# Performance work log

Measured on AMD Instinct MI355X. Metric: run time of the kernel, lower is better.

The kernel has to match this reference:

```python
import jax, jax.numpy as jnp
import numpy as np

POOLING_COUNTS = [15, 8, 8]
N_GRID = 64


def _build_plan(pooling_counts, n):
    """Return list of (kernel_size, conv_stride, i_idx, j_idx) matching torch module order."""
    plan = []
    stride, offset = 1, 0
    for gi, c in enumerate(pooling_counts):
        for k in range(c):
            offset += stride
            i = np.arange(0, n - offset, stride)
            j = np.arange(offset, n, stride)
            ksz = 3 if (gi > 0 and k == 0) else 2
            cstride = 2 if ksz == 3 else 1
            plan.append((ksz, cstride, i, j))
        stride *= 2
    return plan


def _conv1d(x, w, b, stride):
    # x: [B, C, L], w: [O, I, K]
    y = jax.lax.conv_general_dilated(
        x, w, window_strides=(stride,), padding='VALID',
        dimension_numbers=('NCH', 'OIH', 'NCH'))
    return y + b[None, :, None]


def setup_inputs() -> dict:
    key = jax.random.key(0)
    ks = jax.random.split(key, 5)
    H = 256
    x = jax.random.normal(ks[0], (32, H, N_GRID), dtype=jnp.float32)
    w2 = jax.random.normal(ks[1], (29, H, H, 2), dtype=jnp.float32) * 0.03
    b2 = jnp.zeros((29, H), dtype=jnp.float32)
    w3 = jax.random.normal(ks[2], (2, H, H, 3), dtype=jnp.float32) * 0.03
    b3 = jnp.zeros((2, H), dtype=jnp.float32)
    vis_w = jax.random.normal(ks[3], (H, 3 * H), dtype=jnp.float32) * 0.03
    vis_b = jnp.zeros((H,), dtype=jnp.float32)
    return {"x": x, "w2": w2, "b2": b2, "w3": w3, "b3": b3,
            "vis_w": vis_w, "vis_b": vis_b}


def reference(x, w2, b2, w3, b3, vis_w, vis_b):
    plan = _build_plan(POOLING_COUNTS, N_GRID)
    B, D, n = x.shape
    diag = np.arange(n)
    src = x
    map2d = jnp.zeros((B, 3 * D, n, n), dtype=x.dtype)
    map2d = map2d.at[:, :, diag, diag].set(jnp.tile(x, (1, 3, 1)))
    cur = x
    i2 = i3 = 0
    for ksz, cstride, ii, jj in plan:
        if ksz == 2:
            w, b = w2[i2], b2[i2]; i2 += 1
        else:
            w, b = w3[i3], b3[i3]; i3 += 1
        cur = _conv1d(cur, w, b, cstride)          # [B, D, len(ii)]
        feat = jnp.concatenate([src[:, :, ii], cur, src[:, :, jj]], axis=1)
        map2d = map2d.at[:, :, ii, jj].set(feat)
    # 1x1 Conv2d(3D -> D)
    out = jnp.einsum('bcij,oc->boij', map2d, vis_w) + vis_b[None, :, None, None]
    return out
```

## Files before the change

kernel.cpp:

```cpp
#include <hip/hip_runtime.h>

#define BB 32
#define NSTEP 31
#define CROW 1040
#define CB_STRIDE 266240L
#define XB_STRIDE 16384L
#define PPART 524288L
#define RS 528
#define BUF (64 * RS)

__device__ __constant__ int d_lens[NSTEP] = {63,62,61,60,59,58,57,56,55,54,53,52,51,50,49,
                                             24,23,22,21,20,19,18,17,
                                             8,7,6,5,4,3,2,1};
__device__ __constant__ int d_cb[NSTEP] = {0,63,125,186,246,305,363,420,476,531,585,638,690,741,791,
                                           840,864,887,909,930,950,969,987,
                                           1004,1012,1019,1025,1030,1034,1037,1039};

typedef short v8s __attribute__((ext_vector_type(8)));
typedef float v4f __attribute__((ext_vector_type(4)));

__device__ __forceinline__ unsigned short rne_bf16(float f) {
    unsigned int u = __float_as_uint(f);
    u = (u + 0x7FFFu + ((u >> 16) & 1u)) >> 16;
    return (unsigned short)u;
}

#define MFMA16 __builtin_amdgcn_mfma_f32_16x16x32_bf16

__device__ __forceinline__ void lds_barrier() {
    asm volatile("s_waitcnt lgkmcnt(0)\n\ts_barrier" ::: "memory");
}

__global__ __launch_bounds__(256)
void prep(const float* __restrict__ x, const float* __restrict__ w2,
          const float* __restrict__ w3, const float* __restrict__ vw,
          unsigned short* __restrict__ xb, unsigned short* __restrict__ w2t,
          unsigned short* __restrict__ w3t, unsigned short* __restrict__ vwb)
{
    long idx = (long)blockIdx.x * 256 + threadIdx.x;
    if (idx < 524288) {
        const int ci = idx & 255, l = (idx >> 8) & 63, b = (int)(idx >> 14);
        xb[idx] = rne_bf16(x[((long)b << 14) + ((long)ci << 6) + l]);
        return;
    }
    idx -= 524288;
    if (idx < 3801088) {
        const int ci = idx & 255, k = (idx >> 8) & 1; const long row = idx >> 9;
        w2t[idx] = rne_bf16(w2[row * 512 + ci * 2 + k]);
        return;
    }
    idx -= 3801088;
    if (idx < 393216) {
        const int ci = idx & 255; const long r = idx >> 8;
        const int k = (int)(r % 3); const long row = r / 3;
        w3t[idx] = rne_bf16(w3[row * 768 + ci * 3 + k]);
        return;
    }
    idx -= 393216;
    if (idx < 196608) vwb[idx] = rne_bf16(vw[idx]);
}


template<int KC, int S>
__device__ __forceinline__ void conv_big(
    const unsigned short* __restrict__ Wt, const float* __restrict__ bias,
    const char* in, char* out, unsigned short* __restrict__ Cbp,
    int L, int wave, int nl, int g)
{
    const int wm = wave >> 1;
    const int lg2 = wave & 1;
    const int l0 = lg2 * 32 + nl, l1 = l0 + 16;
    const int lv0 = min(l0, L - 1), lv1 = min(l1, L - 1);

    v4f a00 = {0,0,0,0}, a01 = {0,0,0,0}, a10 = {0,0,0,0}, a11 = {0,0,0,0};
    const unsigned short* A0 = Wt + (size_t)(wm * 32 + nl) * (KC * 256) + g * 8;
    const unsigned short* A1 = A0 + (size_t)16 * (KC * 256);

    #pragma unroll
    for (int c = 0; c < KC; ++c) {
        v8s wf0[8], wf1[8];
        #pragma unroll
        for (int k = 0; k < 8; ++k) {
            wf0[k] = *(const v8s*)(A0 + (c * 8 + k) * 32);
            wf1[k] = *(const v8s*)(A1 + (c * 8 + k) * 32);
        }
        const char* rp0 = in + (lv0 * S + c) * RS + g * 16;
        const char* rp1 = in + (lv1 * S + c) * RS + g * 16;
        #pragma unroll
        for (int k = 0; k < 8; ++k) {
            const v8s b0 = *(const v8s*)(rp0 + k * 64);
            const v8s b1 = *(const v8s*)(rp1 + k * 64);
            a00 = MFMA16(wf0[k], b0, a00, 0, 0, 0);
            a10 = MFMA16(wf1[k], b0, a10, 0, 0, 0);
            a01 = MFMA16(wf0[k], b1, a01, 0, 0, 0);
            a11 = MFMA16(wf1[k], b1, a11, 0, 0, 0);
        }
    }
    const int m0 = wm * 32 + g * 4;
    const float4 bv0 = *(const float4*)(bias + m0);
    const float4 bv1 = *(const float4*)(bias + m0 + 16);
    #pragma unroll
    for (int li = 0; li < 2; ++li) {
        const int l = li ? l1 : l0;
        if (l < L) {
            const v4f aa = li ? a01 : a00;
            const v4f ab = li ? a11 : a10;
            ushort4 p0, p1;
            p0.x = rne_bf16(aa[0] + bv0.x); p0.y = rne_bf16(aa[1] + bv0.y);
            p0.z = rne_bf16(aa[2] + bv0.z); p0.w = rne_bf16(aa[3] + bv0.w);
            p1.x = rne_bf16(ab[0] + bv1.x); p1.y = rne_bf16(ab[1] + bv1.y);
            p1.z = rne_bf16(ab[2] + bv1.z); p1.w = rne_bf16(ab[3] + bv1.w);
            *(ushort4*)(out + l * RS + m0 * 2) = p0;
            *(ushort4*)(out + l * RS + (m0 + 16) * 2) = p1;
            *(ushort4*)(Cbp + (size_t)l * 256 + m0) = p0;
            *(ushort4*)(Cbp + (size_t)l * 256 + m0 + 16) = p1;
        }
    }
}

template<int KC, int S, bool TWO_L>
__device__ __forceinline__ void conv_small(
    const unsigned short* __restrict__ Wt, const float* __restrict__ bias,
    const char* in, char* out, unsigned short* __restrict__ Cbp,
    int L, int wave, int nl, int g)
{
    const int lv0 = min(nl, L - 1);
    const int lv1 = min(16 + nl, L - 1);

    v4f a0 = {0,0,0,0}, a1 = {0,0,0,0};
    const unsigned short* A0 = Wt + (size_t)(wave * 16 + nl) * (KC * 256) + g * 8;

    #pragma unroll
    for (int c = 0; c < KC; ++c) {
        v8s wf[8];
        #pragma unroll
        for (int k = 0; k < 8; ++k)
            wf[k] = *(const v8s*)(A0 + (c * 8 + k) * 32);
        const char* rp0 = in + (lv0 * S + c) * RS + g * 16;
        const char* rp1 = in + (lv1 * S + c) * RS + g * 16;
        #pragma unroll
        for (int k = 0; k < 8; ++k) {
            const v8s b0 = *(const v8s*)(rp0 + k * 64);
            a0 = MFMA16(wf[k], b0, a0, 0, 0, 0);
            if (TWO_L) {
                const v8s b1 = *(const v8s*)(rp1 + k * 64);
                a1 = MFMA16(wf[k], b1, a1, 0, 0, 0);
            }
        }
    }
    const int m0 = wave * 16 + g * 4;
    const float4 bv = *(const float4*)(bias + m0);
    {
        const int l = nl;
        if (l < L) {
            ushort4 pk;
            pk.x = rne_bf16(a0[0] + bv.x); pk.y = rne_bf16(a0[1] + bv.y);
            pk.z = rne_bf16(a0[2] + bv.z); pk.w = rne_bf16(a0[3] + bv.w);
            *(ushort4*)(out + l * RS + m0 * 2) = pk;
            *(ushort4*)(Cbp + (size_t)l * 256 + m0) = pk;
        }
    }
    if (TWO_L) {
        const int l = 16 + nl;
        if (l < L) {
            ushort4 pk;
            pk.x = rne_bf16(a1[0] + bv.x); pk.y = rne_bf16(a1[1] + bv.y);
            pk.z = rne_bf16(a1[2] + bv.z); pk.w = rne_bf16(a1[3] + bv.w);
            *(ushort4*)(out + l * RS + m0 * 2) = pk;
            *(ushort4*)(Cbp + (size_t)l * 256 + m0) = pk;
        }
    }
}

__global__ __launch_bounds__(1024, 4)
void chain(const unsigned short* __restrict__ xb,
           const unsigned short* __restrict__ w2t,
           const unsigned short* __restrict__ w3t,
           const float* __restrict__ b2, const float* __restrict__ b3,
           unsigned short* __restrict__ Cb)
{
    __shared__ __align__(16) char lds[2 * BUF];
    const int b = blockIdx.x;
    const int tid = threadIdx.x;
    const int wave = tid >> 6, lane = tid & 63, nl = lane & 15, g = lane >> 4;

    char* base = lds;

    {
        const unsigned short* src = xb + (size_t)b * XB_STRIDE;
        #pragma unroll
        for (int i = 0; i < 2; ++i) {
            const int c = tid + i * 1024;
            const int r = c >> 5, cc = c & 31;
            const v8s v = *(const v8s*)(src + r * 256 + cc * 8);
            *(v8s*)(base + r * RS + cc * 16) = v;
        }
    }
    lds_barrier();

    unsigned short* Cbb = Cb + (size_t)b * CB_STRIDE;
    int cur = 0, i2 = 0, i3 = 0;
    for (int t = 0; t < NSTEP; ++t) {
        const int L = d_lens[t];
        char* inb  = base + cur * BUF;
        char* outb = base + (cur ^ 1) * BUF;
        unsigned short* Cbp = Cbb + (size_t)d_cb[t] * 256;
        if (t < 15) {
            conv_big<2, 1>(w2t + (size_t)i2 * 131072, b2 + i2 * 256,
                           inb, outb, Cbp, L, wave, nl, g);
            ++i2;
        } else if (t == 15) {
            conv_small<3, 2, true>(w3t, b3, inb, outb, Cbp, L, wave, nl, g);
            ++i3;
        } else if (t < 23) {
            conv_small<2, 1, true>(w2t + (size_t)i2 * 131072, b2 + i2 * 256,
                                   inb, outb, Cbp, L, wave, nl, g);
            ++i2;
        } else if (t == 23) {
            conv_small<3, 2, false>(w3t + 196608, b3 + 256,
                                    inb, outb, Cbp, L, wave, nl, g);
            ++i3;
        } else {
            conv_small<2, 1, false>(w2t + (size_t)i2 * 131072, b2 + i2 * 256,
                                    inb, outb, Cbp, L, wave, nl, g);
            ++i2;
        }
        lds_barrier();
        cur ^= 1;
    }
}

template<int OMODE>
__global__ __launch_bounds__(256)
void mg(const unsigned short* __restrict__ A, int arow, int acol0,
        const unsigned short* __restrict__ B, long bbstr,
        void* __restrict__ OUT)
{
    const int lane = threadIdx.x & 63;
    const int wave = threadIdx.x >> 6;
    const int nl = lane & 15, g = lane >> 4;
    const int n = blockIdx.x * 16 + nl;
    const int b = n & 31;
    const int l = n >> 5;
    const int p = blockIdx.y;

    const unsigned short* Ab = A + (size_t)(wave * 64 + nl) * arow + acol0 + p * 256 + g * 8;
    const unsigned short* Bb = B + (size_t)b * bbstr + (size_t)l * 256 + g * 8;

    v4f acc[4] = {};
    #pragma unroll
    for (int k = 0; k < 8; ++k) {
        const v8s bf = *(const v8s*)(Bb + k * 32);
        #pragma unroll
        for (int mf = 0; mf < 4; ++mf) {
            const v8s af = *(const v8s*)(Ab + (size_t)mf * 16 * arow + k * 32);
            acc[mf] = MFMA16(af, bf, acc[mf], 0, 0, 0);
        }
    }
    #pragma unroll
    for (int mf = 0; mf < 4; ++mf) {
        const int m0 = wave * 64 + mf * 16 + g * 4;
        if constexpr (OMODE == 1) {
            *(v4f*)((float*)OUT + (size_t)b * CB_STRIDE + (size_t)l * 256 + m0) = acc[mf];
        } else {
            float* Po = (float*)OUT + (size_t)p * PPART + (size_t)b * XB_STRIDE + l;
            #pragma unroll
            for (int r = 0; r < 4; ++r) Po[(size_t)(m0 + r) * 64] = acc[mf][r];
        }
    }
}

__global__ __launch_bounds__(256)
void final_k(const float* __restrict__ P, const float* __restrict__ Qb,
             const float* __restrict__ vb, float* __restrict__ out)
{
    const int b = blockIdx.x >> 6;
    const int i = blockIdx.x & 63;
    const int t = threadIdx.x;
    const int j = t & 63;
    const int os = t >> 6;

    __shared__ int qidx[64];
    if (t < 64) {
        const int d = t - i;
        int v = -1;
        if (t == i) v = -2;
        else if (d >= 1 && d <= 15) v = d_cb[d-1] + i;
        else if (d >= 17 && d <= 31 && (d & 1) && !(i & 1)) v = d_cb[15 + ((d-17)>>1)] + (i>>1);
        else if (d >= 35 && d <= 63 && ((d-35)&3)==0 && !(i&3)) v = d_cb[23 + ((d-35)>>2)] + (i>>2);
        qidx[t] = v;
    }
    __syncthreads();
    const int q = qidx[j];

    for (int oc = 0; oc < 64; ++oc) {
        const int o = oc * 4 + os;
        const float pl = P[(size_t)(b * 256 + o) * 64 + i];
        const float pm = P[524288u + (size_t)(b * 256 + o) * 64 + i];
        const float* pr = P + 1048576u + (size_t)(b * 256 + o) * 64;
        const float vbv = vb[o];
        float v;
        if (q == -2)      v = pl + pm + pr[i] + vbv;
        else if (q >= 0)  v = pl + Qb[(size_t)b * CB_STRIDE + (size_t)q * 256 + o] + pr[j] + vbv;
        else              v = vbv;
        out[(((size_t)b * 256 + o) * 64 + i) * 64 + j] = v;
    }
}

extern "C" void kernel_launch(void* const* d_in, const int* in_sizes, int n_in,
                              void* d_out, int out_size, void* d_ws, size_t ws_size,
                              hipStream_t stream)
{
    const float* x   = (const float*)d_in[0];
    const float* w2  = (const float*)d_in[1];
    const float* b2  = (const float*)d_in[2];
    const float* w3  = (const float*)d_in[3];
    const float* b3  = (const float*)d_in[4];
    const float* vw  = (const float*)d_in[5];
    const float* vb  = (const float*)d_in[6];
    float* out = (float*)d_out;

    char* w = (char*)d_ws;
    float*          Qf  = (float*)w;          w += (size_t)BB * CB_STRIDE * 4;
    float*          P   = (float*)w;          w += (size_t)3 * PPART * 4;
    unsigned short* Cb  = (unsigned short*)w; w += (size_t)BB * CB_STRIDE * 2;
    unsigned short* xb  = (unsigned short*)w; w += (size_t)BB * XB_STRIDE * 2;
    unsigned short* w2t = (unsigned short*)w; w += (size_t)29 * 131072 * 2;
    unsigned short* w3t = (unsigned short*)w; w += (size_t)2 * 196608 * 2;
    unsigned short* vwb = (unsigned short*)w;

    prep<<<dim3(19200), 256, 0, stream>>>(x, w2, w3, vw, xb, w2t, w3t, vwb);
    mg<2><<<dim3(128, 3), 256, 0, stream>>>(vwb, 768, 0, xb, XB_STRIDE, P);
    chain<<<dim3(BB), 1024, 0, stream>>>(xb, w2t, w3t, b2, b3, Cb);
    mg<1><<<dim3(2080, 1), 256, 0, stream>>>(vwb, 768, 256, Cb, CB_STRIDE, Qf);
    final_k<<<dim3(BB * 64), 256, 0, stream>>>(P, Qf, vb, out);
}
```

Measured before the change: 635.3 us.

## Halve chain block to 512 threads with double-buffered inline-asm weight loads

The sequential conv chain kernel now runs 8 waves per batch block instead of 16. Each wave computes a larger output tile (64 channels × 32 positions for the big steps, 32 channels for the small ones), which raises reuse of the LDS activation fragments. Weight fragments are fetched with inline-asm global loads into two register buffers, using explicit vmcnt waits, so the next chunk's loads overlap the current MFMAs. The cost is more register pressure per wave and fewer waves to hide latency. The chain kernel only launches 32 blocks and is latency-bound.

```diff
diff --git a/kernel.cpp b/kernel.cpp
--- a/kernel.cpp
+++ b/kernel.cpp
@@ -27,6 +27,15 @@
 
 #define MFMA16 __builtin_amdgcn_mfma_f32_16x16x32_bf16
 
+__device__ __forceinline__ v8s gld(const unsigned short* p) {
+    v8s r;
+    asm volatile("global_load_dwordx4 %0, %1, off" : "=v"(r) : "v"(p));
+    return r;
+}
+#define WAIT_VM(N) do { \
+    asm volatile("s_waitcnt vmcnt(" #N ")" ::: "memory"); \
+    __builtin_amdgcn_sched_barrier(0); } while (0)
+
 __device__ __forceinline__ void lds_barrier() {
     asm volatile("s_waitcnt lgkmcnt(0)\n\ts_barrier" ::: "memory");
 }
@@ -61,64 +70,108 @@
 }
 
 
-template<int KC, int S>
+__device__ __forceinline__ void big_issue(v8s (&wf)[8],
+    const unsigned short* const (&A)[4], int kfg0)
+{
+    #pragma unroll
+    for (int kf = 0; kf < 2; ++kf)
+        #pragma unroll
+        for (int c = 0; c < 4; ++c)
+            wf[kf * 4 + c] = gld(A[c] + (kfg0 + kf) * 32);
+}
+__device__ __forceinline__ void big_compute(const v8s (&wf)[8], int kfg0,
+    const char* r0, const char* r1, v4f (&acc)[4][2])
+{
+    #pragma unroll
+    for (int kf = 0; kf < 2; ++kf) {
+        const int kfg = kfg0 + kf;
+        const int kc = kfg >> 3, ko = (kfg & 7) * 64;
+        const v8s b0 = *(const v8s*)(r0 + kc * RS + ko);
+        const v8s b1 = *(const v8s*)(r1 + kc * RS + ko);
+        #pragma unroll
+        for (int c = 0; c < 4; ++c) {
+            acc[c][0] = MFMA16(wf[kf * 4 + c], b0, acc[c][0], 0, 0, 0);
+            acc[c][1] = MFMA16(wf[kf * 4 + c], b1, acc[c][1], 0, 0, 0);
+        }
+    }
+}
 __device__ __forceinline__ void conv_big(
     const unsigned short* __restrict__ Wt, const float* __restrict__ bias,
     const char* in, char* out, unsigned short* __restrict__ Cbp,
     int L, int wave, int nl, int g)
 {
-    const int wm = wave >> 1;
-    const int lg2 = wave & 1;
-    const int l0 = lg2 * 32 + nl, l1 = l0 + 16;
+    const int cb = wave >> 1, lp = wave & 1;
+    const int l0 = lp * 32 + nl, l1 = l0 + 16;
     const int lv0 = min(l0, L - 1), lv1 = min(l1, L - 1);
-
-    v4f a00 = {0,0,0,0}, a01 = {0,0,0,0}, a10 = {0,0,0,0}, a11 = {0,0,0,0};
-    const unsigned short* A0 = Wt + (size_t)(wm * 32 + nl) * (KC * 256) + g * 8;
-    const unsigned short* A1 = A0 + (size_t)16 * (KC * 256);
-
-    #pragma unroll
-    for (int c = 0; c < KC; ++c) {
-        v8s wf0[8], wf1[8];
-        #pragma unroll
-        for (int k = 0; k < 8; ++k) {
-            wf0[k] = *(const v8s*)(A0 + (c * 8 + k) * 32);
-            wf1[k] = *(const v8s*)(A1 + (c * 8 + k) * 32);
-        }
-        const char* rp0 = in + (lv0 * S + c) * RS + g * 16;
-        const char* rp1 = in + (lv1 * S + c) * RS + g * 16;
-        #pragma unroll
-        for (int k = 0; k < 8; ++k) {
-            const v8s b0 = *(const v8s*)(rp0 + k * 64);
-            const v8s b1 = *(const v8s*)(rp1 + k * 64);
-            a00 = MFMA16(wf0[k], b0, a00, 0, 0, 0);
-            a10 = MFMA16(wf1[k], b0, a10, 0, 0, 0);
-            a01 = MFMA16(wf0[k], b1, a01, 0, 0, 0);
-            a11 = MFMA16(wf1[k], b1, a11, 0, 0, 0);
-        }
-    }
-    const int m0 = wm * 32 + g * 4;
-    const float4 bv0 = *(const float4*)(bias + m0);
-    const float4 bv1 = *(const float4*)(bias + m0 + 16);
-    #pragma unroll
-    for (int li = 0; li < 2; ++li) {
-        const int l = li ? l1 : l0;
-        if (l < L) {
-            const v4f aa = li ? a01 : a00;
-            const v4f ab = li ? a11 : a10;
-            ushort4 p0, p1;
-            p0.x = rne_bf16(aa[0] + bv0.x); p0.y = rne_bf16(aa[1] + bv0.y);
-            p0.z = rne_bf16(aa[2] + bv0.z); p0.w = rne_bf16(aa[3] + bv0.w);
-            p1.x = rne_bf16(ab[0] + bv1.x); p1.y = rne_bf16(ab[1] + bv1.y);
-            p1.z = rne_bf16(ab[2] + bv1.z); p1.w = rne_bf16(ab[3] + bv1.w);
-            *(ushort4*)(out + l * RS + m0 * 2) = p0;
-            *(ushort4*)(out + l * RS + (m0 + 16) * 2) = p1;
-            *(ushort4*)(Cbp + (size_t)l * 256 + m0) = p0;
-            *(ushort4*)(Cbp + (size_t)l * 256 + m0 + 16) = p1;
-        }
-    }
-}
-
-template<int KC, int S, bool TWO_L>
+    const unsigned short* A[4];
+    #pragma unroll
+    for (int c = 0; c < 4; ++c)
+        A[c] = Wt + (size_t)(cb * 64 + c * 16 + nl) * 512 + g * 8;
+    const char* r0 = in + lv0 * RS + g * 16;
+    const char* r1 = in + lv1 * RS + g * 16;
+
+    v4f acc[4][2] = {};
+    v8s wA[8], wB[8];
+    big_issue(wA, A, 0);
+    #pragma unroll
+    for (int bp = 0; bp < 4; ++bp) {
+        big_issue(wB, A, bp * 4 + 2);
+        WAIT_VM(8);
+        big_compute(wA, bp * 4, r0, r1, acc);
+        if (bp < 3) { big_issue(wA, A, bp * 4 + 4); WAIT_VM(8); }
+        else        { WAIT_VM(0); }
+        big_compute(wB, bp * 4 + 2, r0, r1, acc);
+    }
+    #pragma unroll
+    for (int c = 0; c < 4; ++c) {
+        const int ch = cb * 64 + c * 16 + g * 4;
+        const float4 bv = *(const float4*)(bias + ch);
+        #pragma unroll
+        for (int li = 0; li < 2; ++li) {
+            const int l = li ? l1 : l0;
+            if (l < L) {
+                const v4f a = acc[c][li];
+                ushort4 pk;
+                pk.x = rne_bf16(a[0] + bv.x); pk.y = rne_bf16(a[1] + bv.y);
+                pk.z = rne_bf16(a[2] + bv.z); pk.w = rne_bf16(a[3] + bv.w);
+                *(ushort4*)(out + l * RS + ch * 2) = pk;
+                *(ushort4*)(Cbp + (size_t)l * 256 + ch) = pk;
+            }
+        }
+    }
+}
+
+template<int KC>
+__device__ __forceinline__ void small_issue(v8s (&wf)[8],
+    const unsigned short* const (&A)[2], int kfg0)
+{
+    #pragma unroll
+    for (int kf = 0; kf < 4; ++kf)
+        #pragma unroll
+        for (int c = 0; c < 2; ++c)
+            wf[kf * 2 + c] = gld(A[c] + (kfg0 + kf) * 32);
+}
+template<int NT>
+__device__ __forceinline__ void small_compute(const v8s (&wf)[8], int kfg0,
+    const char* r0, const char* r1, v4f (&acc)[2][2])
+{
+    #pragma unroll
+    for (int kf = 0; kf < 4; ++kf) {
+        const int kfg = kfg0 + kf;
+        const int kc = kfg >> 3, ko = (kfg & 7) * 64;
+        const v8s b0 = *(const v8s*)(r0 + kc * RS + ko);
+        #pragma unroll
+        for (int c = 0; c < 2; ++c)
+            acc[c][0] = MFMA16(wf[kf * 2 + c], b0, acc[c][0], 0, 0, 0);
+        if (NT > 1) {
+            const v8s b1 = *(const v8s*)(r1 + kc * RS + ko);
+            #pragma unroll
+            for (int c = 0; c < 2; ++c)
+                acc[c][1] = MFMA16(wf[kf * 2 + c], b1, acc[c][1], 0, 0, 0);
+        }
+    }
+}
+template<int KC, int S, int NT>
 __device__ __forceinline__ void conv_small(
     const unsigned short* __restrict__ Wt, const float* __restrict__ bias,
     const char* in, char* out, unsigned short* __restrict__ Cbp,
@@ -126,53 +179,45 @@
 {
     const int lv0 = min(nl, L - 1);
     const int lv1 = min(16 + nl, L - 1);
-
-    v4f a0 = {0,0,0,0}, a1 = {0,0,0,0};
-    const unsigned short* A0 = Wt + (size_t)(wave * 16 + nl) * (KC * 256) + g * 8;
-
-    #pragma unroll
-    for (int c = 0; c < KC; ++c) {
-        v8s wf[8];
-        #pragma unroll
-        for (int k = 0; k < 8; ++k)
-            wf[k] = *(const v8s*)(A0 + (c * 8 + k) * 32);
-        const char* rp0 = in + (lv0 * S + c) * RS + g * 16;
-        const char* rp1 = in + (lv1 * S + c) * RS + g * 16;
-        #pragma unroll
-        for (int k = 0; k < 8; ++k) {
-            const v8s b0 = *(const v8s*)(rp0 + k * 64);
-            a0 = MFMA16(wf[k], b0, a0, 0, 0, 0);
-            if (TWO_L) {
-                const v8s b1 = *(const v8s*)(rp1 + k * 64);
-                a1 = MFMA16(wf[k], b1, a1, 0, 0, 0);
+    const unsigned short* A[2];
+    #pragma unroll
+    for (int c = 0; c < 2; ++c)
+        A[c] = Wt + (size_t)(wave * 32 + c * 16 + nl) * (KC * 256) + g * 8;
+    const char* r0 = in + lv0 * S * RS + g * 16;
+    const char* r1 = in + lv1 * S * RS + g * 16;
+
+    v4f acc[2][2] = {};
+    v8s wA[8], wB[8];
+    small_issue<KC>(wA, A, 0);
+    #pragma unroll
+    for (int bp = 0; bp < KC; ++bp) {
+        small_issue<KC>(wB, A, bp * 8 + 4);
+        WAIT_VM(8);
+        small_compute<NT>(wA, bp * 8, r0, r1, acc);
+        if (bp < KC - 1) { small_issue<KC>(wA, A, bp * 8 + 8); WAIT_VM(8); }
+        else             { WAIT_VM(0); }
+        small_compute<NT>(wB, bp * 8 + 4, r0, r1, acc);
+    }
+    #pragma unroll
+    for (int c = 0; c < 2; ++c) {
+        const int ch = wave * 32 + c * 16 + g * 4;
+        const float4 bv = *(const float4*)(bias + ch);
+        #pragma unroll
+        for (int li = 0; li < NT; ++li) {
+            const int l = li * 16 + nl;
+            if (l < L) {
+                const v4f a = acc[c][li];
+                ushort4 pk;
+                pk.x = rne_bf16(a[0] + bv.x); pk.y = rne_bf16(a[1] + bv.y);
+                pk.z = rne_bf16(a[2] + bv.z); pk.w = rne_bf16(a[3] + bv.w);
+                *(ushort4*)(out + l * RS + ch * 2) = pk;
+                *(ushort4*)(Cbp + (size_t)l * 256 + ch) = pk;
             }
         }
     }
-    const int m0 = wave * 16 + g * 4;
-    const float4 bv = *(const float4*)(bias + m0);
-    {
-        const int l = nl;
-        if (l < L) {
-            ushort4 pk;
-            pk.x = rne_bf16(a0[0] + bv.x); pk.y = rne_bf16(a0[1] + bv.y);
-            pk.z = rne_bf16(a0[2] + bv.z); pk.w = rne_bf16(a0[3] + bv.w);
-            *(ushort4*)(out + l * RS + m0 * 2) = pk;
-            *(ushort4*)(Cbp + (size_t)l * 256 + m0) = pk;
-        }
-    }
-    if (TWO_L) {
-        const int l = 16 + nl;
-        if (l < L) {
-            ushort4 pk;
-            pk.x = rne_bf16(a1[0] + bv.x); pk.y = rne_bf16(a1[1] + bv.y);
-            pk.z = rne_bf16(a1[2] + bv.z); pk.w = rne_bf16(a1[3] + bv.w);
-            *(ushort4*)(out + l * RS + m0 * 2) = pk;
-            *(ushort4*)(Cbp + (size_t)l * 256 + m0) = pk;
-        }
-    }
-}
-
-__global__ __launch_bounds__(1024, 4)
+}
+
+__global__ __launch_bounds__(512, 2)
 void chain(const unsigned short* __restrict__ xb,
            const unsigned short* __restrict__ w2t,
            const unsigned short* __restrict__ w3t,
@@ -189,8 +234,8 @@
     {
         const unsigned short* src = xb + (size_t)b * XB_STRIDE;
         #pragma unroll
-        for (int i = 0; i < 2; ++i) {
-            const int c = tid + i * 1024;
+        for (int i = 0; i < 4; ++i) {
+            const int c = tid + i * 512;
             const int r = c >> 5, cc = c & 31;
             const v8s v = *(const v8s*)(src + r * 256 + cc * 8);
             *(v8s*)(base + r * RS + cc * 16) = v;
@@ -206,23 +251,23 @@
         char* outb = base + (cur ^ 1) * BUF;
         unsigned short* Cbp = Cbb + (size_t)d_cb[t] * 256;
         if (t < 15) {
-            conv_big<2, 1>(w2t + (size_t)i2 * 131072, b2 + i2 * 256,
-                           inb, outb, Cbp, L, wave, nl, g);
+            conv_big(w2t + (size_t)i2 * 131072, b2 + i2 * 256,
+                     inb, outb, Cbp, L, wave, nl, g);
             ++i2;
         } else if (t == 15) {
-            conv_small<3, 2, true>(w3t, b3, inb, outb, Cbp, L, wave, nl, g);
+            conv_small<3, 2, 2>(w3t, b3, inb, outb, Cbp, L, wave, nl, g);
             ++i3;
         } else if (t < 23) {
-            conv_small<2, 1, true>(w2t + (size_t)i2 * 131072, b2 + i2 * 256,
-                                   inb, outb, Cbp, L, wave, nl, g);
+            conv_small<2, 1, 2>(w2t + (size_t)i2 * 131072, b2 + i2 * 256,
+                                inb, outb, Cbp, L, wave, nl, g);
             ++i2;
         } else if (t == 23) {
-            conv_small<3, 2, false>(w3t + 196608, b3 + 256,
-                                    inb, outb, Cbp, L, wave, nl, g);
+            conv_small<3, 2, 1>(w3t + 196608, b3 + 256,
+                                inb, outb, Cbp, L, wave, nl, g);
             ++i3;
         } else {
-            conv_small<2, 1, false>(w2t + (size_t)i2 * 131072, b2 + i2 * 256,
-                                    inb, outb, Cbp, L, wave, nl, g);
+            conv_small<2, 1, 1>(w2t + (size_t)i2 * 131072, b2 + i2 * 256,
+                                inb, outb, Cbp, L, wave, nl, g);
             ++i2;
         }
         lds_barrier();
@@ -331,7 +376,7 @@
 
     prep<<<dim3(19200), 256, 0, stream>>>(x, w2, w3, vw, xb, w2t, w3t, vwb);
     mg<2><<<dim3(128, 3), 256, 0, stream>>>(vwb, 768, 0, xb, XB_STRIDE, P);
-    chain<<<dim3(BB), 1024, 0, stream>>>(xb, w2t, w3t, b2, b3, Cb);
+    chain<<<dim3(BB), 512, 0, stream>>>(xb, w2t, w3t, b2, b3, Cb);
     mg<1><<<dim3(2080, 1), 256, 0, stream>>>(vwb, 768, 256, Cb, CB_STRIDE, Qf);
     final_k<<<dim3(BB * 64), 256, 0, stream>>>(P, Qf, vb, out);
 }
```

Result: slower. 662.3 us (+4.3%).
